# Kernel tuning notes

Measured on AMD Instinct MI355X. Metric: run time of the kernel, lower is better.

Reference implementation:

```python
import jax, jax.numpy as jnp
import numpy as np

D_MODEL = 1024
H = 16
D_K = 64
D_V = 64
D_HALF = D_MODEL // 2  # after_forget == after_summary dims


def setup_inputs() -> dict:
    key = jax.random.key(0)
    ks = jax.random.split(key, 16)
    B, NQ, NK = 2, 2048, 2048
    inp = {
        "queries": jax.random.normal(ks[0], (B, NQ, D_MODEL), jnp.float32),
        "keys": jax.random.normal(ks[1], (B, NK, D_MODEL), jnp.float32),
        "values": jax.random.normal(ks[2], (B, NK, D_MODEL), jnp.float32),
        "attn_mask": jax.random.randint(ks[3], (B, H, NQ, NK), 0, 2).astype(bool),
        "attn_weights": jax.random.uniform(ks[4], (B, H, NQ, NK), jnp.float32),
        # forget-gate linears (torch Linear: y = x @ W.T + b)
        "Wk_f": jax.random.normal(ks[5], (D_HALF, D_MODEL), jnp.float32) * (1.0 / np.sqrt(D_MODEL)),
        "bk_f": jnp.zeros((D_HALF,), jnp.float32),
        "kf_bias": jax.random.normal(ks[6], (1, 1, D_HALF), jnp.float32) * (1.0 / D_HALF),
        "Wv_f": jax.random.normal(ks[7], (D_HALF, D_MODEL), jnp.float32) * (1.0 / np.sqrt(D_MODEL)),
        "bv_f": jnp.zeros((D_HALF,), jnp.float32),
        "vf_bias": jax.random.normal(ks[8], (1, 1, D_HALF), jnp.float32) * (1.0 / D_HALF),
        # summary units
        "k_sum": jax.random.normal(ks[9], (1, 1, D_HALF), jnp.float32) * (1.0 / D_HALF),
        "v_sum": jax.random.normal(ks[10], (1, 1, D_HALF), jnp.float32) * (1.0 / D_HALF),
        # output projection
        "Wo": jax.random.normal(ks[11], (D_MODEL, H * D_V), jnp.float32) * (1.0 / np.sqrt(H * D_V)),
        "bo": jnp.zeros((D_MODEL,), jnp.float32),
    }
    return inp


def reference(queries, keys, values, attn_mask, attn_weights,
              Wk_f, bk_f, kf_bias, Wv_f, bv_f, vf_bias,
              k_sum, v_sum, Wo, bo):
    B, Nq, _ = queries.shape
    Nk = keys.shape[1]
    # forget-gated halves + broadcast summary halves -> full d_model width
    fk = jax.nn.sigmoid(keys @ Wk_f.T + bk_f + kf_bias)        # [B,Nk,D/2]
    fv = jax.nn.sigmoid(values @ Wv_f.T + bv_f + vf_bias)      # [B,Nk,D/2]
    uk = jnp.concatenate([fk, jnp.broadcast_to(k_sum, (B, Nk, D_HALF))], axis=-1)
    uv = jnp.concatenate([fv, jnp.broadcast_to(v_sum, (B, Nk, D_HALF))], axis=-1)
    q = queries.reshape(B, Nq, H, D_K)
    k = uk.reshape(B, Nk, H, D_K)
    v = uv.reshape(B, Nk, H, D_V)
    scores = jnp.einsum("bqhd,bkhd->bhqk", q, k) / np.sqrt(D_K).astype(np.float32)
    scores = scores * attn_weights
    scores = jnp.where(attn_mask, -jnp.inf, scores)
    probs = jax.nn.softmax(scores, axis=-1)                    # [B,H,Nq,Nk]
    out = jnp.einsum("bhqk,bkhd->bqhd", probs, v).reshape(B, Nq, H * D_V)
    return out @ Wo.T + bo
```

## Files before the change

### kernel.cpp

```cpp
#include <hip/hip_runtime.h>

typedef __attribute__((ext_vector_type(8))) short short8;
typedef __attribute__((ext_vector_type(4))) float f32x4;

__device__ __forceinline__ unsigned short f2bf(float f) {
    unsigned u = __float_as_uint(f);
    u += 0x7fffu + ((u >> 16) & 1u);
    return (unsigned short)(u >> 16);
}

__global__ __launch_bounds__(256) void k_compute_c(const float* __restrict__ Wo,
        const float* __restrict__ bo, const float* __restrict__ vsum, float* __restrict__ c) {
    int w = threadIdx.x >> 6, lane = threadIdx.x & 63;
    int j = blockIdx.x * 4 + w;
    const float* row = Wo + (size_t)j * 1024 + 512;
    float acc = 0.0f;
    #pragma unroll
    for (int i = 0; i < 8; ++i) acc = fmaf(row[lane + 64*i], vsum[lane + 64*i], acc);
    #pragma unroll
    for (int off = 32; off; off >>= 1) acc += __shfl_xor(acc, off);
    if (lane == 0) c[j] = acc + bo[j];
}

__global__ __launch_bounds__(256) void k_convq(const float* __restrict__ q, unsigned short* __restrict__ Qh) {
    int t = blockIdx.x * 256 + threadIdx.x;
    int e = t * 4;
    int c = e & 511;
    int bn = e >> 9;
    float4 v = *reinterpret_cast<const float4*>(q + (size_t)bn * 1024 + c);
    int h = c >> 6, d = c & 63;
    int b = bn >> 11, n = bn & 2047;
    ushort4 o;
    o.x = f2bf(v.x * 0.125f); o.y = f2bf(v.y * 0.125f);
    o.z = f2bf(v.z * 0.125f); o.w = f2bf(v.w * 0.125f);
    *reinterpret_cast<ushort4*>(Qh + (((size_t)(b*8+h) * 2048 + n) * 64 + d)) = o;
}

__global__ __launch_bounds__(256) void k_gate(const float* __restrict__ X, const float* __restrict__ W,
        const float* __restrict__ b1, const float* __restrict__ b2,
        unsigned short* __restrict__ out) {
    __shared__ __align__(16) unsigned short Xs[64*88];
    __shared__ __align__(16) unsigned short Wsh[64*88];
    int t = threadIdx.x;
    int mbase = blockIdx.x * 64, nbase = blockIdx.y * 64;
    int w = t >> 6, lane = t & 63, l = lane & 15, quad = lane >> 4;
    int srow = t >> 2, sk = (t & 3) * 16;
    f32x4 acc[4] = {};
    for (int kk = 0; kk < 1024; kk += 64) {
        const float4* xs = reinterpret_cast<const float4*>(X + (size_t)(mbase+srow)*1024 + kk + sk);
        const float4* wsp = reinterpret_cast<const float4*>(W + (size_t)(nbase+srow)*1024 + kk + sk);
        #pragma unroll
        for (int i = 0; i < 4; ++i) {
            float4 xv = xs[i], wv = wsp[i];
            ushort4 xo, wo;
            xo.x=f2bf(xv.x); xo.y=f2bf(xv.y); xo.z=f2bf(xv.z); xo.w=f2bf(xv.w);
            wo.x=f2bf(wv.x); wo.y=f2bf(wv.y); wo.z=f2bf(wv.z); wo.w=f2bf(wv.w);
            *reinterpret_cast<ushort4*>(&Xs[srow*88 + sk + i*4]) = xo;
            *reinterpret_cast<ushort4*>(&Wsh[srow*88 + sk + i*4]) = wo;
        }
        __syncthreads();
        short8 a0 = *reinterpret_cast<const short8*>(&Xs[(w*16+l)*88 + quad*8]);
        short8 a1 = *reinterpret_cast<const short8*>(&Xs[(w*16+l)*88 + 32 + quad*8]);
        #pragma unroll
        for (int nt = 0; nt < 4; ++nt) {
            short8 bq0 = *reinterpret_cast<const short8*>(&Wsh[(l+16*nt)*88 + quad*8]);
            short8 bq1 = *reinterpret_cast<const short8*>(&Wsh[(l+16*nt)*88 + 32 + quad*8]);
            acc[nt] = __builtin_amdgcn_mfma_f32_16x16x32_bf16(a0, bq0, acc[nt], 0, 0, 0);
            acc[nt] = __builtin_amdgcn_mfma_f32_16x16x32_bf16(a1, bq1, acc[nt], 0, 0, 0);
        }
        __syncthreads();
    }
    #pragma unroll
    for (int nt = 0; nt < 4; ++nt) {
        int col = nbase + l + 16*nt;
        float bias = b1[col] + b2[col];
        #pragma unroll
        for (int reg = 0; reg < 4; ++reg) {
            int m = mbase + w*16 + quad*4 + reg;
            float x = acc[nt][reg] + bias;
            float g = 1.0f / (1.0f + __expf(-x));
            int b = m >> 11, n = m & 2047;
            int h = col >> 6, d = col & 63;
            out[(((size_t)(b*8+h)*2048 + n)*64 + d)] = f2bf(g);
        }
    }
}

__global__ __launch_bounds__(256) void k_vtrans(const unsigned short* __restrict__ Vn,
        unsigned short* __restrict__ Vt) {
    __shared__ __align__(16) unsigned short T[64*72];
    int bh = blockIdx.y;
    int n0 = blockIdx.x * 64;
    int t = threadIdx.x;
    int r = t >> 2, c = (t & 3) * 16;
    const unsigned short* src = Vn + ((size_t)bh*2048 + n0 + r)*64 + c;
    short8 v0 = *reinterpret_cast<const short8*>(src);
    short8 v1 = *reinterpret_cast<const short8*>(src + 8);
    *reinterpret_cast<short8*>(&T[r*72 + c]) = v0;
    *reinterpret_cast<short8*>(&T[r*72 + c + 8]) = v1;
    __syncthreads();
    int d = t >> 2, oc = (t & 3) * 16;
    unsigned short tmp[16];
    #pragma unroll
    for (int j = 0; j < 16; ++j) tmp[j] = T[(oc + j)*72 + d];
    unsigned short* dst = Vt + ((size_t)bh*64 + d)*2048 + n0 + oc;
    *reinterpret_cast<short8*>(dst) = *reinterpret_cast<short8*>(&tmp[0]);
    *reinterpret_cast<short8*>(dst + 8) = *reinterpret_cast<short8*>(&tmp[8]);
}

#define NEGBIG -1e30f
__global__ __launch_bounds__(256) void k_attn(const unsigned short* __restrict__ Qh,
        const unsigned short* __restrict__ Kh, const unsigned short* __restrict__ Vt,
        const float* __restrict__ attw, const int* __restrict__ mask,
        unsigned short* __restrict__ O) {
    __shared__ __align__(16) unsigned short Ps[4*16*88];
    __shared__ __align__(16) float Og[2][16*64];
    __shared__ float Ml[2][2][16];
    int bx = blockIdx.x;
    int qt = bx & 63, h = (bx >> 6) & 7, b = bx >> 9;
    int t = threadIdx.x, w = t >> 6, lane = t & 63, l = lane & 15, quad = lane >> 4;
    int qgrp = w >> 1, kh = w & 1;
    int qbase = qt * 32 + qgrp * 16;
    int bh = b*8 + h;
    const unsigned short* qp = Qh + ((size_t)bh*2048 + qbase + l)*64 + quad*8;
    short8 qf0 = *reinterpret_cast<const short8*>(qp);
    short8 qf1 = *reinterpret_cast<const short8*>(qp + 32);
    float m_r[4], l_r[4];
    f32x4 oacc[4] = {};
    #pragma unroll
    for (int r = 0; r < 4; ++r) { m_r[r] = NEGBIG; l_r[r] = 0.0f; }
    unsigned short* Pw = &Ps[w * 16*88];
    const size_t fbase = ((size_t)((b*16 + h)*2048 + qbase + quad*4))*2048 + l;
    const int khbase = kh * 1024;

    float awA[16], awB[16];
    int   mkA[16], mkB[16];

    #pragma unroll
    for (int reg = 0; reg < 4; ++reg)
        #pragma unroll
        for (int nt = 0; nt < 4; ++nt) {
            size_t off = fbase + (size_t)reg*2048 + khbase + 16*nt;
            awA[reg*4+nt] = attw[off];
            mkA[reg*4+nt] = mask[off];
        }

    auto body = [&](int kbase, float* awc, int* mkc, float* awn, int* mkn, bool pref) {
        if (pref) {
            #pragma unroll
            for (int reg = 0; reg < 4; ++reg)
                #pragma unroll
                for (int nt = 0; nt < 4; ++nt) {
                    size_t off = fbase + (size_t)reg*2048 + (kbase + 64) + 16*nt;
                    awn[reg*4+nt] = attw[off];
                    mkn[reg*4+nt] = mask[off];
                }
        }
        f32x4 s[4] = {};
        #pragma unroll
        for (int nt = 0; nt < 4; ++nt) {
            const unsigned short* kp = Kh + ((size_t)bh*2048 + kbase + l + 16*nt)*64 + quad*8;
            short8 k0 = *reinterpret_cast<const short8*>(kp);
            short8 k1 = *reinterpret_cast<const short8*>(kp + 32);
            s[nt] = __builtin_amdgcn_mfma_f32_16x16x32_bf16(qf0, k0, s[nt], 0, 0, 0);
            s[nt] = __builtin_amdgcn_mfma_f32_16x16x32_bf16(qf1, k1, s[nt], 0, 0, 0);
        }
        float sv[4][4];
        #pragma unroll
        for (int reg = 0; reg < 4; ++reg)
            #pragma unroll
            for (int nt = 0; nt < 4; ++nt)
                sv[nt][reg] = mkc[reg*4+nt] ? NEGBIG : s[nt][reg] * awc[reg*4+nt];
        float alpha[4];
        #pragma unroll
        for (int reg = 0; reg < 4; ++reg) {
            float rm = fmaxf(fmaxf(sv[0][reg], sv[1][reg]), fmaxf(sv[2][reg], sv[3][reg]));
            rm = fmaxf(rm, __shfl_xor(rm, 1));
            rm = fmaxf(rm, __shfl_xor(rm, 2));
            rm = fmaxf(rm, __shfl_xor(rm, 4));
            rm = fmaxf(rm, __shfl_xor(rm, 8));
            float mnew = fmaxf(m_r[reg], rm);
            alpha[reg] = __expf(m_r[reg] - mnew);
            m_r[reg] = mnew;
            float rs = 0.0f;
            #pragma unroll
            for (int nt = 0; nt < 4; ++nt) {
                float p = __expf(sv[nt][reg] - mnew);
                sv[nt][reg] = p;
                rs += p;
            }
            rs += __shfl_xor(rs, 1);
            rs += __shfl_xor(rs, 2);
            rs += __shfl_xor(rs, 4);
            rs += __shfl_xor(rs, 8);
            l_r[reg] = l_r[reg] * alpha[reg] + rs;
        }
        #pragma unroll
        for (int dt = 0; dt < 4; ++dt)
            #pragma unroll
            for (int reg = 0; reg < 4; ++reg)
                oacc[dt][reg] *= alpha[reg];
        #pragma unroll
        for (int reg = 0; reg < 4; ++reg)
            #pragma unroll
            for (int nt = 0; nt < 4; ++nt)
                Pw[(quad*4+reg)*88 + l + 16*nt] = f2bf(sv[nt][reg]);
        __builtin_amdgcn_s_waitcnt(0xC07F);
        short8 pf0 = *reinterpret_cast<const short8*>(&Pw[l*88 + quad*8]);
        short8 pf1 = *reinterpret_cast<const short8*>(&Pw[l*88 + 32 + quad*8]);
        #pragma unroll
        for (int dt = 0; dt < 4; ++dt) {
            const unsigned short* vp = Vt + ((size_t)bh*64 + l + 16*dt)*2048 + kbase + quad*8;
            short8 v0 = *reinterpret_cast<const short8*>(vp);
            short8 v1 = *reinterpret_cast<const short8*>(vp + 32);
            oacc[dt] = __builtin_amdgcn_mfma_f32_16x16x32_bf16(pf0, v0, oacc[dt], 0, 0, 0);
            oacc[dt] = __builtin_amdgcn_mfma_f32_16x16x32_bf16(pf1, v1, oacc[dt], 0, 0, 0);
        }
    };

    for (int i = 0; i < 8; ++i) {
        body(khbase + (2*i)*64,   awA, mkA, awB, mkB, true);
        body(khbase + (2*i+1)*64, awB, mkB, awA, mkA, i < 7);
    }

    if (kh == 1) {
        #pragma unroll
        for (int dt = 0; dt < 4; ++dt)
            #pragma unroll
            for (int reg = 0; reg < 4; ++reg)
                Og[qgrp][(quad*4+reg)*64 + l + 16*dt] = oacc[dt][reg];
        if (l == 0) {
            #pragma unroll
            for (int reg = 0; reg < 4; ++reg) {
                Ml[qgrp][0][quad*4+reg] = m_r[reg];
                Ml[qgrp][1][quad*4+reg] = l_r[reg];
            }
        }
    }
    __syncthreads();
    if (kh == 0) {
        #pragma unroll
        for (int reg = 0; reg < 4; ++reg) {
            int row = quad*4 + reg;
            float m1 = Ml[qgrp][0][row];
            float l1 = Ml[qgrp][1][row];
            float mstar = fmaxf(m_r[reg], m1);
            float a0 = __expf(m_r[reg] - mstar);
            float a1 = __expf(m1 - mstar);
            float inv = 1.0f / (l_r[reg]*a0 + l1*a1);
            int qr = qbase + row;
            #pragma unroll
            for (int dt = 0; dt < 4; ++dt) {
                float v1 = Og[qgrp][row*64 + l + 16*dt];
                float val = (oacc[dt][reg]*a0 + v1*a1) * inv;
                O[((size_t)b*2048 + qr)*512 + h*64 + l + 16*dt] = f2bf(val);
            }
        }
    }
}

__global__ __launch_bounds__(256) void k_proj(const unsigned short* __restrict__ O,
        const float* __restrict__ Wo, const float* __restrict__ c, float* __restrict__ out) {
    __shared__ __align__(16) unsigned short Wsh[64*88];
    int t = threadIdx.x;
    int mb = blockIdx.x * 64, nb = blockIdx.y * 64;
    int w = t >> 6, lane = t & 63, l = lane & 15, quad = lane >> 4;
    int srow = t >> 2, sk = (t & 3) * 16;
    f32x4 acc[4] = {};
    for (int kb = 0; kb < 512; kb += 64) {
        const float4* wp = reinterpret_cast<const float4*>(Wo + (size_t)(nb+srow)*1024 + kb + sk);
        #pragma unroll
        for (int i = 0; i < 4; ++i) {
            float4 wv = wp[i];
            ushort4 wo2;
            wo2.x=f2bf(wv.x); wo2.y=f2bf(wv.y); wo2.z=f2bf(wv.z); wo2.w=f2bf(wv.w);
            *reinterpret_cast<ushort4*>(&Wsh[srow*88 + sk + i*4]) = wo2;
        }
        __syncthreads();
        const unsigned short* op = O + (size_t)(mb + w*16 + l)*512 + kb + quad*8;
        short8 a0 = *reinterpret_cast<const short8*>(op);
        short8 a1 = *reinterpret_cast<const short8*>(op + 32);
        #pragma unroll
        for (int nt = 0; nt < 4; ++nt) {
            short8 b0 = *reinterpret_cast<const short8*>(&Wsh[(l+16*nt)*88 + quad*8]);
            short8 b1 = *reinterpret_cast<const short8*>(&Wsh[(l+16*nt)*88 + 32 + quad*8]);
            acc[nt] = __builtin_amdgcn_mfma_f32_16x16x32_bf16(a0, b0, acc[nt], 0, 0, 0);
            acc[nt] = __builtin_amdgcn_mfma_f32_16x16x32_bf16(a1, b1, acc[nt], 0, 0, 0);
        }
        __syncthreads();
    }
    #pragma unroll
    for (int nt = 0; nt < 4; ++nt) {
        int coln = nb + l + 16*nt;
        float cv = c[coln];
        #pragma unroll
        for (int reg = 0; reg < 4; ++reg) {
            int row = mb + w*16 + quad*4 + reg;
            out[(size_t)row*1024 + coln] = acc[nt][reg] + cv;
        }
    }
}

extern "C" void kernel_launch(void* const* d_in, const int* in_sizes, int n_in,
                              void* d_out, int out_size, void* d_ws, size_t ws_size,
                              hipStream_t stream) {
    const float* queries = (const float*)d_in[0];
    const float* keys    = (const float*)d_in[1];
    const float* values  = (const float*)d_in[2];
    const int*   mask    = (const int*)d_in[3];
    const float* attw    = (const float*)d_in[4];
    const float* Wk_f    = (const float*)d_in[5];
    const float* bk_f    = (const float*)d_in[6];
    const float* kf_bias = (const float*)d_in[7];
    const float* Wv_f    = (const float*)d_in[8];
    const float* bv_f    = (const float*)d_in[9];
    const float* vf_bias = (const float*)d_in[10];
    const float* v_sum   = (const float*)d_in[12];
    const float* Wo      = (const float*)d_in[13];
    const float* bo      = (const float*)d_in[14];
    float* out = (float*)d_out;

    char* ws = (char*)d_ws;
    float* cvec = (float*)ws;
    unsigned short* Qh = (unsigned short*)(ws + 4096);
    unsigned short* Kh = Qh + (size_t)2*8*2048*64;
    unsigned short* Vt = Kh + (size_t)2*8*2048*64;
    unsigned short* Vn = Vt + (size_t)2*8*2048*64;
    unsigned short* Ob = Vn;

    hipLaunchKernelGGL(k_compute_c, dim3(256), dim3(256), 0, stream, Wo, bo, v_sum, cvec);
    hipLaunchKernelGGL(k_convq, dim3(2048), dim3(256), 0, stream, queries, Qh);
    hipLaunchKernelGGL(k_gate, dim3(64, 8), dim3(256), 0, stream, keys, Wk_f, bk_f, kf_bias, Kh);
    hipLaunchKernelGGL(k_gate, dim3(64, 8), dim3(256), 0, stream, values, Wv_f, bv_f, vf_bias, Vn);
    hipLaunchKernelGGL(k_vtrans, dim3(32, 16), dim3(256), 0, stream, Vn, Vt);
    hipLaunchKernelGGL(k_attn, dim3(1024), dim3(256), 0, stream, Qh, Kh, Vt, attw, mask, Ob);
    hipLaunchKernelGGL(k_proj, dim3(64, 16), dim3(256), 0, stream, Ob, Wo, cvec, out);
}
```

Before: 1.093 ms.

## Merge prep kernels into one launch, fuse V transpose, pre-convert Wo to bf16

Five preprocessing kernels (Q conversion, the two gate GEMMs, the V transpose and the bias-vector computation) become one block-indexed kernel. The V transpose now happens in the gate epilogue through shared memory, which removes the separate Vn round trip. The gate GEMM gains register prefetch of the next k-tile, and Wo is converted to bf16 once so k_proj reads bf16 directly from global memory without LDS staging or barriers. This cuts launch overhead and redundant traffic. The cost is a more heterogeneous single kernel and uncoalesced-ish direct global B loads in the projection.

```diff
diff --git a/kernel.cpp b/kernel.cpp
--- a/kernel.cpp
+++ b/kernel.cpp
@@ -9,103 +9,141 @@
     return (unsigned short)(u >> 16);
 }
 
-__global__ __launch_bounds__(256) void k_compute_c(const float* __restrict__ Wo,
-        const float* __restrict__ bo, const float* __restrict__ vsum, float* __restrict__ c) {
-    int w = threadIdx.x >> 6, lane = threadIdx.x & 63;
-    int j = blockIdx.x * 4 + w;
-    const float* row = Wo + (size_t)j * 1024 + 512;
-    float acc = 0.0f;
-    #pragma unroll
-    for (int i = 0; i < 8; ++i) acc = fmaf(row[lane + 64*i], vsum[lane + 64*i], acc);
-    #pragma unroll
-    for (int off = 32; off; off >>= 1) acc += __shfl_xor(acc, off);
-    if (lane == 0) c[j] = acc + bo[j];
-}
-
-__global__ __launch_bounds__(256) void k_convq(const float* __restrict__ q, unsigned short* __restrict__ Qh) {
-    int t = blockIdx.x * 256 + threadIdx.x;
-    int e = t * 4;
-    int c = e & 511;
-    int bn = e >> 9;
-    float4 v = *reinterpret_cast<const float4*>(q + (size_t)bn * 1024 + c);
-    int h = c >> 6, d = c & 63;
-    int b = bn >> 11, n = bn & 2047;
-    ushort4 o;
-    o.x = f2bf(v.x * 0.125f); o.y = f2bf(v.y * 0.125f);
-    o.z = f2bf(v.z * 0.125f); o.w = f2bf(v.w * 0.125f);
-    *reinterpret_cast<ushort4*>(Qh + (((size_t)(b*8+h) * 2048 + n) * 64 + d)) = o;
-}
-
-__global__ __launch_bounds__(256) void k_gate(const float* __restrict__ X, const float* __restrict__ W,
-        const float* __restrict__ b1, const float* __restrict__ b2,
-        unsigned short* __restrict__ out) {
-    __shared__ __align__(16) unsigned short Xs[64*88];
-    __shared__ __align__(16) unsigned short Wsh[64*88];
+__global__ __launch_bounds__(256) void k_prep(
+        const float* __restrict__ queries,
+        const float* __restrict__ keys, const float* __restrict__ values,
+        const float* __restrict__ Wk_f, const float* __restrict__ bk_f, const float* __restrict__ kf_bias,
+        const float* __restrict__ Wv_f, const float* __restrict__ bv_f, const float* __restrict__ vf_bias,
+        const float* __restrict__ Wo, const float* __restrict__ bo, const float* __restrict__ vsum,
+        unsigned short* __restrict__ Qh, unsigned short* __restrict__ Kh,
+        unsigned short* __restrict__ Vt, unsigned short* __restrict__ Wob,
+        float* __restrict__ cvec) {
+    __shared__ __align__(16) unsigned short SMEM[11264];
+    int bx = blockIdx.x;
     int t = threadIdx.x;
-    int mbase = blockIdx.x * 64, nbase = blockIdx.y * 64;
-    int w = t >> 6, lane = t & 63, l = lane & 15, quad = lane >> 4;
-    int srow = t >> 2, sk = (t & 3) * 16;
-    f32x4 acc[4] = {};
-    for (int kk = 0; kk < 1024; kk += 64) {
-        const float4* xs = reinterpret_cast<const float4*>(X + (size_t)(mbase+srow)*1024 + kk + sk);
-        const float4* wsp = reinterpret_cast<const float4*>(W + (size_t)(nbase+srow)*1024 + kk + sk);
+
+    if (bx < 2048) {
+        int e = (bx * 256 + t) * 4;
+        int c = e & 511;
+        int bn = e >> 9;
+        float4 v = *reinterpret_cast<const float4*>(queries + (size_t)bn * 1024 + c);
+        int h = c >> 6, d = c & 63;
+        int b = bn >> 11, n = bn & 2047;
+        ushort4 o;
+        o.x = f2bf(v.x * 0.125f); o.y = f2bf(v.y * 0.125f);
+        o.z = f2bf(v.z * 0.125f); o.w = f2bf(v.w * 0.125f);
+        *reinterpret_cast<ushort4*>(Qh + (((size_t)(b*8+h) * 2048 + n) * 64 + d)) = o;
+    } else if (bx < 3072) {
+        bool isK = bx < 2560;
+        int local = bx - (isK ? 2048 : 2560);
+        int mb = local & 63, by = local >> 6;
+        const float* X  = isK ? keys : values;
+        const float* W  = isK ? Wk_f : Wv_f;
+        const float* b1 = isK ? bk_f : bv_f;
+        const float* b2 = isK ? kf_bias : vf_bias;
+        unsigned short* Xs  = SMEM;
+        unsigned short* Wsh = SMEM + 5632;
+        int mbase = mb * 64, nbase = by * 64;
+        int w = t >> 6, lane = t & 63, l = lane & 15, quad = lane >> 4;
+        int srow = t >> 2, sk = (t & 3) * 16;
+        const float* Xrow = X + (size_t)(mbase + srow) * 1024 + sk;
+        const float* Wrow = W + (size_t)(nbase + srow) * 1024 + sk;
+        float4 xr[4], wr[4];
         #pragma unroll
         for (int i = 0; i < 4; ++i) {
-            float4 xv = xs[i], wv = wsp[i];
-            ushort4 xo, wo;
-            xo.x=f2bf(xv.x); xo.y=f2bf(xv.y); xo.z=f2bf(xv.z); xo.w=f2bf(xv.w);
-            wo.x=f2bf(wv.x); wo.y=f2bf(wv.y); wo.z=f2bf(wv.z); wo.w=f2bf(wv.w);
-            *reinterpret_cast<ushort4*>(&Xs[srow*88 + sk + i*4]) = xo;
-            *reinterpret_cast<ushort4*>(&Wsh[srow*88 + sk + i*4]) = wo;
-        }
-        __syncthreads();
-        short8 a0 = *reinterpret_cast<const short8*>(&Xs[(w*16+l)*88 + quad*8]);
-        short8 a1 = *reinterpret_cast<const short8*>(&Xs[(w*16+l)*88 + 32 + quad*8]);
-        #pragma unroll
-        for (int nt = 0; nt < 4; ++nt) {
-            short8 bq0 = *reinterpret_cast<const short8*>(&Wsh[(l+16*nt)*88 + quad*8]);
-            short8 bq1 = *reinterpret_cast<const short8*>(&Wsh[(l+16*nt)*88 + 32 + quad*8]);
-            acc[nt] = __builtin_amdgcn_mfma_f32_16x16x32_bf16(a0, bq0, acc[nt], 0, 0, 0);
-            acc[nt] = __builtin_amdgcn_mfma_f32_16x16x32_bf16(a1, bq1, acc[nt], 0, 0, 0);
-        }
-        __syncthreads();
-    }
-    #pragma unroll
-    for (int nt = 0; nt < 4; ++nt) {
-        int col = nbase + l + 16*nt;
-        float bias = b1[col] + b2[col];
-        #pragma unroll
-        for (int reg = 0; reg < 4; ++reg) {
-            int m = mbase + w*16 + quad*4 + reg;
-            float x = acc[nt][reg] + bias;
-            float g = 1.0f / (1.0f + __expf(-x));
-            int b = m >> 11, n = m & 2047;
-            int h = col >> 6, d = col & 63;
-            out[(((size_t)(b*8+h)*2048 + n)*64 + d)] = f2bf(g);
-        }
-    }
-}
-
-__global__ __launch_bounds__(256) void k_vtrans(const unsigned short* __restrict__ Vn,
-        unsigned short* __restrict__ Vt) {
-    __shared__ __align__(16) unsigned short T[64*72];
-    int bh = blockIdx.y;
-    int n0 = blockIdx.x * 64;
-    int t = threadIdx.x;
-    int r = t >> 2, c = (t & 3) * 16;
-    const unsigned short* src = Vn + ((size_t)bh*2048 + n0 + r)*64 + c;
-    short8 v0 = *reinterpret_cast<const short8*>(src);
-    short8 v1 = *reinterpret_cast<const short8*>(src + 8);
-    *reinterpret_cast<short8*>(&T[r*72 + c]) = v0;
-    *reinterpret_cast<short8*>(&T[r*72 + c + 8]) = v1;
-    __syncthreads();
-    int d = t >> 2, oc = (t & 3) * 16;
-    unsigned short tmp[16];
-    #pragma unroll
-    for (int j = 0; j < 16; ++j) tmp[j] = T[(oc + j)*72 + d];
-    unsigned short* dst = Vt + ((size_t)bh*64 + d)*2048 + n0 + oc;
-    *reinterpret_cast<short8*>(dst) = *reinterpret_cast<short8*>(&tmp[0]);
-    *reinterpret_cast<short8*>(dst + 8) = *reinterpret_cast<short8*>(&tmp[8]);
+            xr[i] = *reinterpret_cast<const float4*>(Xrow + i*4);
+            wr[i] = *reinterpret_cast<const float4*>(Wrow + i*4);
+        }
+        f32x4 acc[4] = {};
+        for (int kk = 0; kk < 1024; kk += 64) {
+            #pragma unroll
+            for (int i = 0; i < 4; ++i) {
+                float4 xv = xr[i], wv = wr[i];
+                ushort4 xo, wo;
+                xo.x=f2bf(xv.x); xo.y=f2bf(xv.y); xo.z=f2bf(xv.z); xo.w=f2bf(xv.w);
+                wo.x=f2bf(wv.x); wo.y=f2bf(wv.y); wo.z=f2bf(wv.z); wo.w=f2bf(wv.w);
+                *reinterpret_cast<ushort4*>(&Xs[srow*88 + sk + i*4]) = xo;
+                *reinterpret_cast<ushort4*>(&Wsh[srow*88 + sk + i*4]) = wo;
+            }
+            __syncthreads();
+            if (kk + 64 < 1024) {
+                #pragma unroll
+                for (int i = 0; i < 4; ++i) {
+                    xr[i] = *reinterpret_cast<const float4*>(Xrow + kk + 64 + i*4);
+                    wr[i] = *reinterpret_cast<const float4*>(Wrow + kk + 64 + i*4);
+                }
+            }
+            short8 a0 = *reinterpret_cast<const short8*>(&Xs[(w*16+l)*88 + quad*8]);
+            short8 a1 = *reinterpret_cast<const short8*>(&Xs[(w*16+l)*88 + 32 + quad*8]);
+            #pragma unroll
+            for (int nt = 0; nt < 4; ++nt) {
+                short8 bq0 = *reinterpret_cast<const short8*>(&Wsh[(l+16*nt)*88 + quad*8]);
+                short8 bq1 = *reinterpret_cast<const short8*>(&Wsh[(l+16*nt)*88 + 32 + quad*8]);
+                acc[nt] = __builtin_amdgcn_mfma_f32_16x16x32_bf16(a0, bq0, acc[nt], 0, 0, 0);
+                acc[nt] = __builtin_amdgcn_mfma_f32_16x16x32_bf16(a1, bq1, acc[nt], 0, 0, 0);
+            }
+            __syncthreads();
+        }
+        if (isK) {
+            #pragma unroll
+            for (int nt = 0; nt < 4; ++nt) {
+                int col = nbase + l + 16*nt;
+                float bias = b1[col] + b2[col];
+                #pragma unroll
+                for (int reg = 0; reg < 4; ++reg) {
+                    int m = mbase + w*16 + quad*4 + reg;
+                    float x = acc[nt][reg] + bias;
+                    float g = 1.0f / (1.0f + __expf(-x));
+                    int bb = m >> 11, n = m & 2047;
+                    int hh = col >> 6, d = col & 63;
+                    Kh[(((size_t)(bb*8+hh)*2048 + n)*64 + d)] = f2bf(g);
+                }
+            }
+        } else {
+            unsigned short* Ts = SMEM;
+            #pragma unroll
+            for (int nt = 0; nt < 4; ++nt) {
+                int col = nbase + l + 16*nt;
+                float bias = b1[col] + b2[col];
+                #pragma unroll
+                for (int reg = 0; reg < 4; ++reg) {
+                    float x = acc[nt][reg] + bias;
+                    float g = 1.0f / (1.0f + __expf(-x));
+                    Ts[(w*16 + quad*4 + reg)*72 + (l + 16*nt)] = f2bf(g);
+                }
+            }
+            __syncthreads();
+            int d = t >> 2, c4 = (t & 3) * 16;
+            unsigned short tmp[16];
+            #pragma unroll
+            for (int j = 0; j < 16; ++j) tmp[j] = Ts[(c4 + j)*72 + d];
+            int bb = mbase >> 11, n0 = mbase & 2047;
+            unsigned short* dst = Vt + ((size_t)(bb*8+by)*64 + d)*2048 + n0 + c4;
+            *reinterpret_cast<short8*>(dst)     = *reinterpret_cast<short8*>(&tmp[0]);
+            *reinterpret_cast<short8*>(dst + 8) = *reinterpret_cast<short8*>(&tmp[8]);
+        }
+    } else if (bx < 3328) {
+        int w = t >> 6, lane = t & 63;
+        int j = (bx - 3072) * 4 + w;
+        const float* row = Wo + (size_t)j * 1024 + 512;
+        float acc = 0.0f;
+        #pragma unroll
+        for (int i = 0; i < 8; ++i) acc = fmaf(row[lane + 64*i], vsum[lane + 64*i], acc);
+        #pragma unroll
+        for (int off = 32; off; off >>= 1) acc += __shfl_xor(acc, off);
+        if (lane == 0) cvec[j] = acc + bo[j];
+    } else {
+        int base = ((bx - 3328) * 256 + t) * 16;
+        int row = base >> 9, col = base & 511;
+        const float4* src = reinterpret_cast<const float4*>(Wo + (size_t)row * 1024 + col);
+        #pragma unroll
+        for (int i = 0; i < 4; ++i) {
+            float4 v = src[i];
+            ushort4 o;
+            o.x=f2bf(v.x); o.y=f2bf(v.y); o.z=f2bf(v.z); o.w=f2bf(v.w);
+            *reinterpret_cast<ushort4*>(Wob + base + i*4) = o;
+        }
+    }
 }
 
 #define NEGBIG -1e30f
@@ -260,34 +298,23 @@
 }
 
 __global__ __launch_bounds__(256) void k_proj(const unsigned short* __restrict__ O,
-        const float* __restrict__ Wo, const float* __restrict__ c, float* __restrict__ out) {
-    __shared__ __align__(16) unsigned short Wsh[64*88];
+        const unsigned short* __restrict__ Wob, const float* __restrict__ c, float* __restrict__ out) {
     int t = threadIdx.x;
     int mb = blockIdx.x * 64, nb = blockIdx.y * 64;
     int w = t >> 6, lane = t & 63, l = lane & 15, quad = lane >> 4;
-    int srow = t >> 2, sk = (t & 3) * 16;
+    const unsigned short* op = O + (size_t)(mb + w*16 + l)*512 + quad*8;
+    const unsigned short* wp = Wob + (size_t)(nb + l)*512 + quad*8;
     f32x4 acc[4] = {};
     for (int kb = 0; kb < 512; kb += 64) {
-        const float4* wp = reinterpret_cast<const float4*>(Wo + (size_t)(nb+srow)*1024 + kb + sk);
-        #pragma unroll
-        for (int i = 0; i < 4; ++i) {
-            float4 wv = wp[i];
-            ushort4 wo2;
-            wo2.x=f2bf(wv.x); wo2.y=f2bf(wv.y); wo2.z=f2bf(wv.z); wo2.w=f2bf(wv.w);
-            *reinterpret_cast<ushort4*>(&Wsh[srow*88 + sk + i*4]) = wo2;
-        }
-        __syncthreads();
-        const unsigned short* op = O + (size_t)(mb + w*16 + l)*512 + kb + quad*8;
-        short8 a0 = *reinterpret_cast<const short8*>(op);
-        short8 a1 = *reinterpret_cast<const short8*>(op + 32);
+        short8 a0 = *reinterpret_cast<const short8*>(op + kb);
+        short8 a1 = *reinterpret_cast<const short8*>(op + kb + 32);
         #pragma unroll
         for (int nt = 0; nt < 4; ++nt) {
-            short8 b0 = *reinterpret_cast<const short8*>(&Wsh[(l+16*nt)*88 + quad*8]);
-            short8 b1 = *reinterpret_cast<const short8*>(&Wsh[(l+16*nt)*88 + 32 + quad*8]);
+            short8 b0 = *reinterpret_cast<const short8*>(wp + nt*16*512 + kb);
+            short8 b1 = *reinterpret_cast<const short8*>(wp + nt*16*512 + kb + 32);
             acc[nt] = __builtin_amdgcn_mfma_f32_16x16x32_bf16(a0, b0, acc[nt], 0, 0, 0);
             acc[nt] = __builtin_amdgcn_mfma_f32_16x16x32_bf16(a1, b1, acc[nt], 0, 0, 0);
         }
-        __syncthreads();
     }
     #pragma unroll
     for (int nt = 0; nt < 4; ++nt) {
@@ -322,17 +349,15 @@
 
     char* ws = (char*)d_ws;
     float* cvec = (float*)ws;
-    unsigned short* Qh = (unsigned short*)(ws + 4096);
-    unsigned short* Kh = Qh + (size_t)2*8*2048*64;
-    unsigned short* Vt = Kh + (size_t)2*8*2048*64;
-    unsigned short* Vn = Vt + (size_t)2*8*2048*64;
-    unsigned short* Ob = Vn;
-
-    hipLaunchKernelGGL(k_compute_c, dim3(256), dim3(256), 0, stream, Wo, bo, v_sum, cvec);
-    hipLaunchKernelGGL(k_convq, dim3(2048), dim3(256), 0, stream, queries, Qh);
-    hipLaunchKernelGGL(k_gate, dim3(64, 8), dim3(256), 0, stream, keys, Wk_f, bk_f, kf_bias, Kh);
-    hipLaunchKernelGGL(k_gate, dim3(64, 8), dim3(256), 0, stream, values, Wv_f, bv_f, vf_bias, Vn);
-    hipLaunchKernelGGL(k_vtrans, dim3(32, 16), dim3(256), 0, stream, Vn, Vt);
+    unsigned short* Qh  = (unsigned short*)(ws + 4096);
+    unsigned short* Kh  = Qh + (size_t)2*8*2048*64;
+    unsigned short* Vt  = Kh + (size_t)2*8*2048*64;
+    unsigned short* Ob  = Vt + (size_t)2*8*2048*64;
+    unsigned short* Wob = Ob + (size_t)2*8*2048*64;
+
+    hipLaunchKernelGGL(k_prep, dim3(3456), dim3(256), 0, stream,
+        queries, keys, values, Wk_f, bk_f, kf_bias, Wv_f, bv_f, vf_bias,
+        Wo, bo, v_sum, Qh, Kh, Vt, Wob, cvec);
     hipLaunchKernelGGL(k_attn, dim3(1024), dim3(256), 0, stream, Qh, Kh, Vt, attw, mask, Ob);
-    hipLaunchKernelGGL(k_proj, dim3(64, 16), dim3(256), 0, stream, Ob, Wo, cvec, out);
-}
+    hipLaunchKernelGGL(k_proj, dim3(64, 16), dim3(256), 0, stream, Ob, Wob, cvec, out);
+}
```

After: 1.097 ms. About the same (+0.3%).
